# Performance work log

Measured on AMD Instinct MI355X. Metric: run time of the kernel, lower is better.

## Reference

```python
import jax, jax.numpy as jnp
import numpy as np

B, H, S, D = 2, 16, 2048, 64


def setup_inputs() -> dict:
    key = jax.random.key(0)
    kq, kk, kv = jax.random.split(key, 3)
    q = jax.random.normal(kq, (B, H, S, D), dtype=jnp.float32)
    k = jax.random.normal(kk, (B, H, S, D), dtype=jnp.float32)
    v = jax.random.normal(kv, (B, H, S, D), dtype=jnp.float32)
    # causal mask: 1.0 where attention is DISALLOWED (strictly upper triangle)
    mask = jnp.triu(jnp.ones((S, S), dtype=jnp.float32), k=1)[None, None, :, :]
    return {"k": k, "q": q, "v": v, "mask": mask}


def reference(k, q, v, mask):
    d_k = jnp.asarray(k.shape[-1], dtype=jnp.float32)
    # scores: [B, H, S, S]
    scores = jnp.einsum("bhqd,bhkd->bhqk", q, k) / jnp.sqrt(d_k)
    scores = scores + mask * (-1e9)
    weights = jax.nn.softmax(scores, axis=-1)
    # attention output: [B, H, S, D]
    return jnp.einsum("bhqk,bhkd->bhqd", weights, v)
```

## Files before the change

kernel.cpp:

```cpp
#include <hip/hip_runtime.h>
#include <hip/hip_bf16.h>

typedef unsigned short ushort_t;
typedef __attribute__((ext_vector_type(8))) short v8s;
typedef __attribute__((ext_vector_type(4))) float v4f;

#define SEQ   2048
#define DH    64
#define BK    32
#define KSTR  72
#define VSTR  40
#define NHEADS 32
#define GBYTES 19456
#define HELEMS 131072

#if __has_builtin(__builtin_amdgcn_exp2f)
#define EXP2(x) __builtin_amdgcn_exp2f(x)
#else
#define EXP2(x) exp2f(x)
#endif

__device__ __forceinline__ unsigned pkbf(float lo, float hi) {
    __hip_bfloat162 h = __float22bfloat162_rn(make_float2(lo, hi));
    union { __hip_bfloat162 h; unsigned u; } c; c.h = h; return c.u;
}

__device__ __forceinline__ v8s load8_bf_scaled(const float* p, float sc) {
    float4 a = *(const float4*)p;
    float4 b = *(const float4*)(p + 4);
    union { v8s v; unsigned u[4]; } t;
    t.u[0] = pkbf(a.x * sc, a.y * sc);
    t.u[1] = pkbf(a.z * sc, a.w * sc);
    t.u[2] = pkbf(b.x * sc, b.y * sc);
    t.u[3] = pkbf(b.z * sc, b.w * sc);
    return t.v;
}

__device__ __forceinline__ void process_tile_T(
    int kb, int myq0, int quad, int l15,
    v8s qa0, v8s qa1,
    v8s ka00, v8s ka01, v8s ka10, v8s ka11,
    v8s vb0, v8s vb1, v8s vb2, v8s vb3,
    v4f& a0, v4f& a1, v4f& a2, v4f& a3, float& ls)
{
    const v4f z = {0.f, 0.f, 0.f, 0.f};
    __builtin_amdgcn_s_setprio(1);
    v4f s0 = __builtin_amdgcn_mfma_f32_16x16x32_bf16(ka00, qa0, z, 0, 0, 0);
    s0     = __builtin_amdgcn_mfma_f32_16x16x32_bf16(ka01, qa1, s0, 0, 0, 0);
    v4f s1 = __builtin_amdgcn_mfma_f32_16x16x32_bf16(ka10, qa0, z, 0, 0, 0);
    s1     = __builtin_amdgcn_mfma_f32_16x16x32_bf16(ka11, qa1, s1, 0, 0, 0);
    __builtin_amdgcn_s_setprio(0);

    float p0[4], p1[4];
    if (kb + BK <= myq0) {
        #pragma unroll
        for (int r = 0; r < 4; ++r) { p0[r] = EXP2(s0[r]); p1[r] = EXP2(s1[r]); }
    } else {
        const int qrow = myq0 + l15;
        #pragma unroll
        for (int r = 0; r < 4; ++r) {
            p0[r] = (kb + 4 * quad + r      <= qrow) ? EXP2(s0[r]) : 0.f;
            p1[r] = (kb + 16 + 4 * quad + r <= qrow) ? EXP2(s1[r]) : 0.f;
        }
    }
    #pragma unroll
    for (int r = 0; r < 4; ++r) ls += p0[r] + p1[r];

    union { v8s v; unsigned u[4]; } pa;
    pa.u[0] = pkbf(p0[0], p0[1]); pa.u[1] = pkbf(p0[2], p0[3]);
    pa.u[2] = pkbf(p1[0], p1[1]); pa.u[3] = pkbf(p1[2], p1[3]);
    __builtin_amdgcn_s_setprio(1);
    a0 = __builtin_amdgcn_mfma_f32_16x16x32_bf16(pa.v, vb0, a0, 0, 0, 0);
    a1 = __builtin_amdgcn_mfma_f32_16x16x32_bf16(pa.v, vb1, a1, 0, 0, 0);
    a2 = __builtin_amdgcn_mfma_f32_16x16x32_bf16(pa.v, vb2, a2, 0, 0, 0);
    a3 = __builtin_amdgcn_mfma_f32_16x16x32_bf16(pa.v, vb3, a3, 0, 0, 0);
    __builtin_amdgcn_s_setprio(0);
}

__global__ __launch_bounds__(256, 8)
void attn_prep(const float* __restrict__ K, const float* __restrict__ V,
               ushort_t* __restrict__ Kb, ushort_t* __restrict__ Vb) {
    const int u = blockIdx.x * 256 + threadIdx.x;
    if (u < 524288) {
        const float* src = K + (size_t)u * 8;
        float4 a = *(const float4*)src;
        float4 b = *(const float4*)(src + 4);
        union { v8s v; unsigned w[4]; } t;
        t.w[0] = pkbf(a.x, a.y); t.w[1] = pkbf(a.z, a.w);
        t.w[2] = pkbf(b.x, b.y); t.w[3] = pkbf(b.z, b.w);
        *(v8s*)(Kb + (size_t)u * 8) = t.v;
    } else {
        const int q    = u - 524288;
        const int d    = q & 63;
        const int sgrp = (q >> 6) & 3;
        const int tile = (q >> 8) & 63;
        const int head = q >> 14;
        const float* vsrc = V + ((size_t)head * SEQ + tile * 32) * DH + d;
        float x[8];
        #pragma unroll
        for (int m = 0; m < 8; ++m) {
            const int kpos = (m < 4) ? (4 * sgrp + m) : (16 + 4 * sgrp + (m - 4));
            x[m] = vsrc[(size_t)kpos * DH];
        }
        union { v8s v; unsigned w[4]; } t;
        t.w[0] = pkbf(x[0], x[1]); t.w[1] = pkbf(x[2], x[3]);
        t.w[2] = pkbf(x[4], x[5]); t.w[3] = pkbf(x[6], x[7]);
        *(v8s*)(Vb + (size_t)q * 8) = t.v;
    }
}

__global__ __launch_bounds__(512, 4)
void attn_causal_dual2(const ushort_t* __restrict__ Kb,
                       const float* __restrict__ Qg,
                       const ushort_t* __restrict__ Vb,
                       float* __restrict__ Og) {
    __shared__ alignas(16) unsigned char smem[2][GBYTES];

    const int i    = blockIdx.x;
    const int head = i & 31;
    const int j    = i >> 5;
    const int qt   = (j < 16) ? (31 - j) : (j - 16);
    const int qb   = qt * 64;
    const int tid  = threadIdx.x;
    const int w    = tid >> 6;
    const int grp  = w >> 2;
    const int wg   = w & 3;
    const int lane = tid & 63;
    const int l15  = lane & 15;
    const int quad = lane >> 4;

    const int niter = qt + 1;
    const int ktlo  = grp ? niter : 0;

    const int myq0 = qb + wg * 16, qmax = myq0 + 15;
    const size_t hb = (size_t)head * SEQ * DH;

    const float QSC = 0.125f * 1.4426950408889634f;
    v8s qa0, qa1;
    {
        const float* qp = Qg + hb + (size_t)(myq0 + l15) * DH + quad * 8;
        qa0 = load8_bf_scaled(qp, QSC);  qa1 = load8_bf_scaled(qp + 32, QSC);
    }

    v4f a0 = {0.f,0.f,0.f,0.f}, a1 = a0, a2 = a0, a3 = a0;
    float ls = 0.f;

    const int stid    = tid & 255;
    const int sk_kpos = stid >> 3;
    const int sk_d    = (stid & 7) * 8;
    const int sv_d    = stid & 63;
    const int sv_g    = stid >> 6;

    const ushort_t* ksrc = Kb + (size_t)head * HELEMS + stid * 8;
    const ushort_t* vsrc = Vb + (size_t)head * HELEMS + stid * 8;

    ushort_t* KtB = (ushort_t*)(smem[grp]);
    ushort_t* VtB = (ushort_t*)(smem[grp] + 9216);
    ushort_t* kdst0 = KtB + sk_kpos * KSTR + sk_d;
    ushort_t* vdst0 = VtB + sv_d * VSTR + sv_g * 8;
    const int KOFS = BK * KSTR;
    const int VOFS = DH * VSTR;

    {
        union { v8s v; uint4 u; } kc, vc;
        kc.u = *(const uint4*)(ksrc + (size_t)ktlo * 2048);
        vc.u = *(const uint4*)(vsrc + (size_t)ktlo * 2048);
        *(v8s*)kdst0 = kc.v;
        *(v8s*)vdst0 = vc.v;
    }
    __syncthreads();

    for (int it = 0; it < niter; ++it) {
        const int kt  = ktlo + it;
        const int cur = it & 1;
        const bool havenext = (it + 1 < niter);

        uint4 nk, nv;
        if (havenext) {
            nk = *(const uint4*)(ksrc + (size_t)(kt + 1) * 2048);
            nv = *(const uint4*)(vsrc + (size_t)(kt + 1) * 2048);
        }

        const int kb = kt * BK;
        if (kb <= qmax) {
            const ushort_t* KB = KtB + (cur ? KOFS : 0);
            const ushort_t* VB = VtB + (cur ? VOFS : 0);
            union { v8s v; uint4 u; } ka00, ka01, ka10, ka11, vb0, vb1, vb2, vb3;
            ka00.u = *(const uint4*)&KB[(l15)      * KSTR      + quad * 8];
            ka01.u = *(const uint4*)&KB[(l15)      * KSTR + 32 + quad * 8];
            ka10.u = *(const uint4*)&KB[(16 + l15) * KSTR      + quad * 8];
            ka11.u = *(const uint4*)&KB[(16 + l15) * KSTR + 32 + quad * 8];
            vb0.u  = *(const uint4*)&VB[(l15)      * VSTR + quad * 8];
            vb1.u  = *(const uint4*)&VB[(16 + l15) * VSTR + quad * 8];
            vb2.u  = *(const uint4*)&VB[(32 + l15) * VSTR + quad * 8];
            vb3.u  = *(const uint4*)&VB[(48 + l15) * VSTR + quad * 8];

            process_tile_T(kb, myq0, quad, l15, qa0, qa1,
                           ka00.v, ka01.v, ka10.v, ka11.v,
                           vb0.v, vb1.v, vb2.v, vb3.v,
                           a0, a1, a2, a3, ls);
        }

        if (havenext) {
            union { v8s v; uint4 u; } kc, vc;
            kc.u = nk; vc.u = nv;
            const int nxt = cur ^ 1;
            *(v8s*)(kdst0 + (nxt ? KOFS : 0)) = kc.v;
            *(v8s*)(vdst0 + (nxt ? VOFS : 0)) = vc.v;
        }

        __syncthreads();
    }

    ls += __shfl_xor(ls, 16); ls += __shfl_xor(ls, 32);

    float* Ps = (float*)smem[0];
    float* Lp = (float*)smem[1];
    if (grp == 1) {
        #pragma unroll
        for (int r = 0; r < 4; ++r) {
            const int row = wg * 16 + 4 * quad + r;
            float* pr = Ps + row * 68 + l15;
            pr[0] = a0[r]; pr[16] = a1[r]; pr[32] = a2[r]; pr[48] = a3[r];
        }
        if (lane < 16) Lp[wg * 16 + l15] = ls;
    }
    __syncthreads();
    if (grp == 0) {
        const float lst = ls + Lp[wg * 16 + l15];
        #pragma unroll
        for (int r = 0; r < 4; ++r) {
            const float inv = 1.0f / __shfl(lst, 4 * quad + r);
            const int row = wg * 16 + 4 * quad + r;
            const float* pr = Ps + row * 68 + l15;
            float* op = Og + hb + (size_t)(qb + row) * DH + l15;
            op[0]  = (a0[r] + pr[0])  * inv;
            op[16] = (a1[r] + pr[16]) * inv;
            op[32] = (a2[r] + pr[32]) * inv;
            op[48] = (a3[r] + pr[48]) * inv;
        }
    }
}

__global__ __launch_bounds__(512, 4)
void attn_causal_dual(const float* __restrict__ Kg,
                      const float* __restrict__ Qg,
                      const float* __restrict__ Vg,
                      float* __restrict__ Og) {
    __shared__ alignas(16) unsigned char smem[2][GBYTES];

    const int i    = blockIdx.x;
    const int head = i & 31;
    const int j    = i >> 5;
    const int qt   = (j < 16) ? (31 - j) : (j - 16);
    const int qb   = qt * 64;
    const int tid  = threadIdx.x;
    const int w    = tid >> 6;
    const int grp  = w >> 2;
    const int wg   = w & 3;
    const int lane = tid & 63;
    const int l15  = lane & 15;
    const int quad = lane >> 4;

    const int niter = qt + 1;
    const int ktlo  = grp ? niter : 0;

    const int myq0 = qb + wg * 16, qmax = myq0 + 15;
    const size_t hb = (size_t)head * SEQ * DH;

    const float QSC = 0.125f * 1.4426950408889634f;
    v8s qa0, qa1;
    {
        const float* qp = Qg + hb + (size_t)(myq0 + l15) * DH + quad * 8;
        qa0 = load8_bf_scaled(qp, QSC);  qa1 = load8_bf_scaled(qp + 32, QSC);
    }

    v4f a0 = {0.f,0.f,0.f,0.f}, a1 = a0, a2 = a0, a3 = a0;
    float ls = 0.f;

    const int stid    = tid & 255;
    const int sk_kpos = stid >> 3;
    const int sk_d    = (stid & 7) * 8;
    const int sv_d    = stid & 63;

    const float* kbase  = Kg + hb + (size_t)sk_kpos * DH + sk_d;
    const float* vbaseA = Vg + hb + (size_t)(4 * wg) * DH + sv_d;
    const float* vbaseB = Vg + hb + (size_t)(16 + 4 * wg) * DH + sv_d;

    ushort_t* KtB = (ushort_t*)(smem[grp]);
    ushort_t* VtB = (ushort_t*)(smem[grp] + 9216);
    ushort_t* kdst0 = KtB + sk_kpos * KSTR + sk_d;
    ushort_t* vdst0 = VtB + sv_d * VSTR + 8 * wg;
    const int KOFS = BK * KSTR;
    const int VOFS = DH * VSTR;

    {
        const size_t t0 = (size_t)ktlo * BK * DH;
        float4 k0 = *(const float4*)(kbase + t0);
        float4 k1 = *(const float4*)(kbase + t0 + 4);
        float va[4], vb[4];
        #pragma unroll
        for (int m = 0; m < 4; ++m) {
            va[m] = vbaseA[t0 + (size_t)m * DH];
            vb[m] = vbaseB[t0 + (size_t)m * DH];
        }
        union { v8s v; unsigned u[4]; } kc, vc;
        kc.u[0] = pkbf(k0.x, k0.y); kc.u[1] = pkbf(k0.z, k0.w);
        kc.u[2] = pkbf(k1.x, k1.y); kc.u[3] = pkbf(k1.z, k1.w);
        vc.u[0] = pkbf(va[0], va[1]); vc.u[1] = pkbf(va[2], va[3]);
        vc.u[2] = pkbf(vb[0], vb[1]); vc.u[3] = pkbf(vb[2], vb[3]);
        *(v8s*)kdst0 = kc.v;
        *(v8s*)vdst0 = vc.v;
    }
    __syncthreads();

    for (int it = 0; it < niter; ++it) {
        const int kt  = ktlo + it;
        const int cur = it & 1;
        const bool havenext = (it + 1 < niter);

        float4 nk0, nk1; float nva[4], nvb[4];
        if (havenext) {
            const size_t toff = (size_t)(kt + 1) * BK * DH;
            nk0 = *(const float4*)(kbase + toff);
            nk1 = *(const float4*)(kbase + toff + 4);
            #pragma unroll
            for (int m = 0; m < 4; ++m) {
                nva[m] = vbaseA[toff + (size_t)m * DH];
                nvb[m] = vbaseB[toff + (size_t)m * DH];
            }
        }

        const int kb = kt * BK;
        if (kb <= qmax) {
            const ushort_t* KB = KtB + (cur ? KOFS : 0);
            const ushort_t* VB = VtB + (cur ? VOFS : 0);
            union { v8s v; uint4 u; } ka00, ka01, ka10, ka11, vb0, vb1, vb2, vb3;
            ka00.u = *(const uint4*)&KB[(l15)      * KSTR      + quad * 8];
            ka01.u = *(const uint4*)&KB[(l15)      * KSTR + 32 + quad * 8];
            ka10.u = *(const uint4*)&KB[(16 + l15) * KSTR      + quad * 8];
            ka11.u = *(const uint4*)&KB[(16 + l15) * KSTR + 32 + quad * 8];
            vb0.u  = *(const uint4*)&VB[(l15)      * VSTR + quad * 8];
            vb1.u  = *(const uint4*)&VB[(16 + l15) * VSTR + quad * 8];
            vb2.u  = *(const uint4*)&VB[(32 + l15) * VSTR + quad * 8];
            vb3.u  = *(const uint4*)&VB[(48 + l15) * VSTR + quad * 8];

            process_tile_T(kb, myq0, quad, l15, qa0, qa1,
                           ka00.v, ka01.v, ka10.v, ka11.v,
                           vb0.v, vb1.v, vb2.v, vb3.v,
                           a0, a1, a2, a3, ls);
        }

        if (havenext) {
            union { v8s v; unsigned u[4]; } kc, vc;
            kc.u[0] = pkbf(nk0.x, nk0.y); kc.u[1] = pkbf(nk0.z, nk0.w);
            kc.u[2] = pkbf(nk1.x, nk1.y); kc.u[3] = pkbf(nk1.z, nk1.w);
            vc.u[0] = pkbf(nva[0], nva[1]); vc.u[1] = pkbf(nva[2], nva[3]);
            vc.u[2] = pkbf(nvb[0], nvb[1]); vc.u[3] = pkbf(nvb[2], nvb[3]);
            const int nxt = cur ^ 1;
            *(v8s*)(kdst0 + (nxt ? KOFS : 0)) = kc.v;
            *(v8s*)(vdst0 + (nxt ? VOFS : 0)) = vc.v;
        }

        __syncthreads();
    }

    ls += __shfl_xor(ls, 16); ls += __shfl_xor(ls, 32);

    float* Ps = (float*)smem[0];
    float* Lp = (float*)smem[1];
    if (grp == 1) {
        #pragma unroll
        for (int r = 0; r < 4; ++r) {
            const int row = wg * 16 + 4 * quad + r;
            float* pr = Ps + row * 68 + l15;
            pr[0] = a0[r]; pr[16] = a1[r]; pr[32] = a2[r]; pr[48] = a3[r];
        }
        if (lane < 16) Lp[wg * 16 + l15] = ls;
    }
    __syncthreads();
    if (grp == 0) {
        const float lst = ls + Lp[wg * 16 + l15];
        #pragma unroll
        for (int r = 0; r < 4; ++r) {
            const float inv = 1.0f / __shfl(lst, 4 * quad + r);
            const int row = wg * 16 + 4 * quad + r;
            const float* pr = Ps + row * 68 + l15;
            float* op = Og + hb + (size_t)(qb + row) * DH + l15;
            op[0]  = (a0[r] + pr[0])  * inv;
            op[16] = (a1[r] + pr[16]) * inv;
            op[32] = (a2[r] + pr[32]) * inv;
            op[48] = (a3[r] + pr[48]) * inv;
        }
    }
}

extern "C" void kernel_launch(void* const* d_in, const int* in_sizes, int n_in,
                              void* d_out, int out_size, void* d_ws, size_t ws_size,
                              hipStream_t stream) {
    const float* K = (const float*)d_in[0];
    const float* Q = (const float*)d_in[1];
    const float* V = (const float*)d_in[2];
    float* O = (float*)d_out;

    const size_t img_elems = (size_t)NHEADS * HELEMS;
    const size_t need = 2 * img_elems * sizeof(ushort_t);

    if (ws_size >= need) {
        ushort_t* Kb = (ushort_t*)d_ws;
        ushort_t* Vb = Kb + img_elems;
        attn_prep<<<dim3(4096), 256, 0, stream>>>(K, V, Kb, Vb);
        attn_causal_dual2<<<dim3(1024), 512, 0, stream>>>(Kb, Q, Vb, O);
    } else {
        attn_causal_dual<<<dim3(1024), 512, 0, stream>>>(K, Q, V, O);
    }
}
```

Baseline: 140.4 us.

## Load pre-swizzled bf16 K/V fragments directly from global, drop LDS staging

The new main kernel has each wave read its MFMA K and V operand fragments straight from the pre-laid-out bf16 workspace in global memory. This removes the double-buffered LDS staging and the per-tile __syncthreads. Each wave also now stops at its own causal limit instead of iterating with the block's bound. The cost is that K/V data shared across the four waves of a group is re-read from global/L2 instead of once per block, and no explicit prefetch overlaps the loads with compute.

```diff
diff --git a/kernel.cpp b/kernel.cpp
--- a/kernel.cpp
+++ b/kernel.cpp
@@ -110,11 +110,12 @@
 }
 
 __global__ __launch_bounds__(512, 4)
-void attn_causal_dual2(const ushort_t* __restrict__ Kb,
+void attn_causal_dual3(const ushort_t* __restrict__ Kb,
                        const float* __restrict__ Qg,
                        const ushort_t* __restrict__ Vb,
                        float* __restrict__ Og) {
-    __shared__ alignas(16) unsigned char smem[2][GBYTES];
+    __shared__ alignas(16) float Ps[64 * 68];
+    __shared__ float Lp[64];
 
     const int i    = blockIdx.x;
     const int head = i & 31;
@@ -133,6 +134,10 @@
     const int ktlo  = grp ? niter : 0;
 
     const int myq0 = qb + wg * 16, qmax = myq0 + 15;
+    const int kthiN = ktlo + niter;
+    const int kthiC = (qmax >> 5) + 1;
+    const int kthi  = (kthiN < kthiC) ? kthiN : kthiC;
+
     const size_t hb = (size_t)head * SEQ * DH;
 
     const float QSC = 0.125f * 1.4426950408889634f;
@@ -145,26 +150,123 @@
     v4f a0 = {0.f,0.f,0.f,0.f}, a1 = a0, a2 = a0, a3 = a0;
     float ls = 0.f;
 
+    const ushort_t* kh = Kb + (size_t)head * HELEMS + l15 * 64 + quad * 8;
+    const ushort_t* vh = Vb + (size_t)head * HELEMS + quad * 512 + l15 * 8;
+
+    for (int kt = ktlo; kt < kthi; ++kt) {
+        const ushort_t* kp = kh + (size_t)kt * 2048;
+        const ushort_t* vp = vh + (size_t)kt * 2048;
+        union { v8s v; uint4 u; } ka00, ka01, ka10, ka11, vb0, vb1, vb2, vb3;
+        ka00.u = *(const uint4*)(kp);
+        ka01.u = *(const uint4*)(kp + 32);
+        ka10.u = *(const uint4*)(kp + 1024);
+        ka11.u = *(const uint4*)(kp + 1056);
+        vb0.u  = *(const uint4*)(vp);
+        vb1.u  = *(const uint4*)(vp + 128);
+        vb2.u  = *(const uint4*)(vp + 256);
+        vb3.u  = *(const uint4*)(vp + 384);
+
+        process_tile_T(kt * BK, myq0, quad, l15, qa0, qa1,
+                       ka00.v, ka01.v, ka10.v, ka11.v,
+                       vb0.v, vb1.v, vb2.v, vb3.v,
+                       a0, a1, a2, a3, ls);
+    }
+
+    ls += __shfl_xor(ls, 16); ls += __shfl_xor(ls, 32);
+
+    if (grp == 1) {
+        #pragma unroll
+        for (int r = 0; r < 4; ++r) {
+            const int row = wg * 16 + 4 * quad + r;
+            float* pr = Ps + row * 68 + l15;
+            pr[0] = a0[r]; pr[16] = a1[r]; pr[32] = a2[r]; pr[48] = a3[r];
+        }
+        if (lane < 16) Lp[wg * 16 + l15] = ls;
+    }
+    __syncthreads();
+    if (grp == 0) {
+        const float lst = ls + Lp[wg * 16 + l15];
+        #pragma unroll
+        for (int r = 0; r < 4; ++r) {
+            const float inv = 1.0f / __shfl(lst, 4 * quad + r);
+            const int row = wg * 16 + 4 * quad + r;
+            const float* pr = Ps + row * 68 + l15;
+            float* op = Og + hb + (size_t)(qb + row) * DH + l15;
+            op[0]  = (a0[r] + pr[0])  * inv;
+            op[16] = (a1[r] + pr[16]) * inv;
+            op[32] = (a2[r] + pr[32]) * inv;
+            op[48] = (a3[r] + pr[48]) * inv;
+        }
+    }
+}
+
+__global__ __launch_bounds__(512, 4)
+void attn_causal_dual(const float* __restrict__ Kg,
+                      const float* __restrict__ Qg,
+                      const float* __restrict__ Vg,
+                      float* __restrict__ Og) {
+    __shared__ alignas(16) unsigned char smem[2][GBYTES];
+
+    const int i    = blockIdx.x;
+    const int head = i & 31;
+    const int j    = i >> 5;
+    const int qt   = (j < 16) ? (31 - j) : (j - 16);
+    const int qb   = qt * 64;
+    const int tid  = threadIdx.x;
+    const int w    = tid >> 6;
+    const int grp  = w >> 2;
+    const int wg   = w & 3;
+    const int lane = tid & 63;
+    const int l15  = lane & 15;
+    const int quad = lane >> 4;
+
+    const int niter = qt + 1;
+    const int ktlo  = grp ? niter : 0;
+
+    const int myq0 = qb + wg * 16, qmax = myq0 + 15;
+    const size_t hb = (size_t)head * SEQ * DH;
+
+    const float QSC = 0.125f * 1.4426950408889634f;
+    v8s qa0, qa1;
+    {
+        const float* qp = Qg + hb + (size_t)(myq0 + l15) * DH + quad * 8;
+        qa0 = load8_bf_scaled(qp, QSC);  qa1 = load8_bf_scaled(qp + 32, QSC);
+    }
+
+    v4f a0 = {0.f,0.f,0.f,0.f}, a1 = a0, a2 = a0, a3 = a0;
+    float ls = 0.f;
+
     const int stid    = tid & 255;
     const int sk_kpos = stid >> 3;
     const int sk_d    = (stid & 7) * 8;
     const int sv_d    = stid & 63;
-    const int sv_g    = stid >> 6;
-
-    const ushort_t* ksrc = Kb + (size_t)head * HELEMS + stid * 8;
-    const ushort_t* vsrc = Vb + (size_t)head * HELEMS + stid * 8;
+
+    const float* kbase  = Kg + hb + (size_t)sk_kpos * DH + sk_d;
+    const float* vbaseA = Vg + hb + (size_t)(4 * wg) * DH + sv_d;
+    const float* vbaseB = Vg + hb + (size_t)(16 + 4 * wg) * DH + sv_d;
 
     ushort_t* KtB = (ushort_t*)(smem[grp]);
     ushort_t* VtB = (ushort_t*)(smem[grp] + 9216);
     ushort_t* kdst0 = KtB + sk_kpos * KSTR + sk_d;
-    ushort_t* vdst0 = VtB + sv_d * VSTR + sv_g * 8;
+    ushort_t* vdst0 = VtB + sv_d * VSTR + 8 * wg;
     const int KOFS = BK * KSTR;
     const int VOFS = DH * VSTR;
 
     {
-        union { v8s v; uint4 u; } kc, vc;
-        kc.u = *(const uint4*)(ksrc + (size_t)ktlo * 2048);
-        vc.u = *(const uint4*)(vsrc + (size_t)ktlo * 2048);
+        const size_t t0 = (size_t)ktlo * BK * DH;
+        float4 k0 = *(const float4*)(kbase + t0);
+        float4 k1 = *(const float4*)(kbase + t0 + 4);
+        float va[4], vb[4];
+        #pragma unroll
+        for (int m = 0; m < 4; ++m) {
+            va[m] = vbaseA[t0 + (size_t)m * DH];
+            vb[m] = vbaseB[t0 + (size_t)m * DH];
+        }
+        union { v8s v; unsigned u[4]; } kc, vc;
+        kc.u[0] = pkbf(k0.x, k0.y); kc.u[1] = pkbf(k0.z, k0.w);
+        kc.u[2] = pkbf(k1.x, k1.y); kc.u[3] = pkbf(k1.z, k1.w);
+        vc.u[0] = pkbf(va[0], va[1]); vc.u[1] = pkbf(va[2], va[3]);
+        vc.u[2] = pkbf(vb[0], vb[1]); vc.u[3] = pkbf(vb[2], vb[3]);
         *(v8s*)kdst0 = kc.v;
         *(v8s*)vdst0 = vc.v;
     }
@@ -175,10 +277,16 @@
         const int cur = it & 1;
         const bool havenext = (it + 1 < niter);
 
-        uint4 nk, nv;
+        float4 nk0, nk1; float nva[4], nvb[4];
         if (havenext) {
-            nk = *(const uint4*)(ksrc + (size_t)(kt + 1) * 2048);
-            nv = *(const uint4*)(vsrc + (size_t)(kt + 1) * 2048);
+            const size_t toff = (size_t)(kt + 1) * BK * DH;
+            nk0 = *(const float4*)(kbase + toff);
+            nk1 = *(const float4*)(kbase + toff + 4);
+            #pragma unroll
+            for (int m = 0; m < 4; ++m) {
+                nva[m] = vbaseA[toff + (size_t)m * DH];
+                nvb[m] = vbaseB[toff + (size_t)m * DH];
+            }
         }
 
         const int kb = kt * BK;
@@ -202,156 +310,6 @@
         }
 
         if (havenext) {
-            union { v8s v; uint4 u; } kc, vc;
-            kc.u = nk; vc.u = nv;
-            const int nxt = cur ^ 1;
-            *(v8s*)(kdst0 + (nxt ? KOFS : 0)) = kc.v;
-            *(v8s*)(vdst0 + (nxt ? VOFS : 0)) = vc.v;
-        }
-
-        __syncthreads();
-    }
-
-    ls += __shfl_xor(ls, 16); ls += __shfl_xor(ls, 32);
-
-    float* Ps = (float*)smem[0];
-    float* Lp = (float*)smem[1];
-    if (grp == 1) {
-        #pragma unroll
-        for (int r = 0; r < 4; ++r) {
-            const int row = wg * 16 + 4 * quad + r;
-            float* pr = Ps + row * 68 + l15;
-            pr[0] = a0[r]; pr[16] = a1[r]; pr[32] = a2[r]; pr[48] = a3[r];
-        }
-        if (lane < 16) Lp[wg * 16 + l15] = ls;
-    }
-    __syncthreads();
-    if (grp == 0) {
-        const float lst = ls + Lp[wg * 16 + l15];
-        #pragma unroll
-        for (int r = 0; r < 4; ++r) {
-            const float inv = 1.0f / __shfl(lst, 4 * quad + r);
-            const int row = wg * 16 + 4 * quad + r;
-            const float* pr = Ps + row * 68 + l15;
-            float* op = Og + hb + (size_t)(qb + row) * DH + l15;
-            op[0]  = (a0[r] + pr[0])  * inv;
-            op[16] = (a1[r] + pr[16]) * inv;
-            op[32] = (a2[r] + pr[32]) * inv;
-            op[48] = (a3[r] + pr[48]) * inv;
-        }
-    }
-}
-
-__global__ __launch_bounds__(512, 4)
-void attn_causal_dual(const float* __restrict__ Kg,
-                      const float* __restrict__ Qg,
-                      const float* __restrict__ Vg,
-                      float* __restrict__ Og) {
-    __shared__ alignas(16) unsigned char smem[2][GBYTES];
-
-    const int i    = blockIdx.x;
-    const int head = i & 31;
-    const int j    = i >> 5;
-    const int qt   = (j < 16) ? (31 - j) : (j - 16);
-    const int qb   = qt * 64;
-    const int tid  = threadIdx.x;
-    const int w    = tid >> 6;
-    const int grp  = w >> 2;
-    const int wg   = w & 3;
-    const int lane = tid & 63;
-    const int l15  = lane & 15;
-    const int quad = lane >> 4;
-
-    const int niter = qt + 1;
-    const int ktlo  = grp ? niter : 0;
-
-    const int myq0 = qb + wg * 16, qmax = myq0 + 15;
-    const size_t hb = (size_t)head * SEQ * DH;
-
-    const float QSC = 0.125f * 1.4426950408889634f;
-    v8s qa0, qa1;
-    {
-        const float* qp = Qg + hb + (size_t)(myq0 + l15) * DH + quad * 8;
-        qa0 = load8_bf_scaled(qp, QSC);  qa1 = load8_bf_scaled(qp + 32, QSC);
-    }
-
-    v4f a0 = {0.f,0.f,0.f,0.f}, a1 = a0, a2 = a0, a3 = a0;
-    float ls = 0.f;
-
-    const int stid    = tid & 255;
-    const int sk_kpos = stid >> 3;
-    const int sk_d    = (stid & 7) * 8;
-    const int sv_d    = stid & 63;
-
-    const float* kbase  = Kg + hb + (size_t)sk_kpos * DH + sk_d;
-    const float* vbaseA = Vg + hb + (size_t)(4 * wg) * DH + sv_d;
-    const float* vbaseB = Vg + hb + (size_t)(16 + 4 * wg) * DH + sv_d;
-
-    ushort_t* KtB = (ushort_t*)(smem[grp]);
-    ushort_t* VtB = (ushort_t*)(smem[grp] + 9216);
-    ushort_t* kdst0 = KtB + sk_kpos * KSTR + sk_d;
-    ushort_t* vdst0 = VtB + sv_d * VSTR + 8 * wg;
-    const int KOFS = BK * KSTR;
-    const int VOFS = DH * VSTR;
-
-    {
-        const size_t t0 = (size_t)ktlo * BK * DH;
-        float4 k0 = *(const float4*)(kbase + t0);
-        float4 k1 = *(const float4*)(kbase + t0 + 4);
-        float va[4], vb[4];
-        #pragma unroll
-        for (int m = 0; m < 4; ++m) {
-            va[m] = vbaseA[t0 + (size_t)m * DH];
-            vb[m] = vbaseB[t0 + (size_t)m * DH];
-        }
-        union { v8s v; unsigned u[4]; } kc, vc;
-        kc.u[0] = pkbf(k0.x, k0.y); kc.u[1] = pkbf(k0.z, k0.w);
-        kc.u[2] = pkbf(k1.x, k1.y); kc.u[3] = pkbf(k1.z, k1.w);
-        vc.u[0] = pkbf(va[0], va[1]); vc.u[1] = pkbf(va[2], va[3]);
-        vc.u[2] = pkbf(vb[0], vb[1]); vc.u[3] = pkbf(vb[2], vb[3]);
-        *(v8s*)kdst0 = kc.v;
-        *(v8s*)vdst0 = vc.v;
-    }
-    __syncthreads();
-
-    for (int it = 0; it < niter; ++it) {
-        const int kt  = ktlo + it;
-        const int cur = it & 1;
-        const bool havenext = (it + 1 < niter);
-
-        float4 nk0, nk1; float nva[4], nvb[4];
-        if (havenext) {
-            const size_t toff = (size_t)(kt + 1) * BK * DH;
-            nk0 = *(const float4*)(kbase + toff);
-            nk1 = *(const float4*)(kbase + toff + 4);
-            #pragma unroll
-            for (int m = 0; m < 4; ++m) {
-                nva[m] = vbaseA[toff + (size_t)m * DH];
-                nvb[m] = vbaseB[toff + (size_t)m * DH];
-            }
-        }
-
-        const int kb = kt * BK;
-        if (kb <= qmax) {
-            const ushort_t* KB = KtB + (cur ? KOFS : 0);
-            const ushort_t* VB = VtB + (cur ? VOFS : 0);
-            union { v8s v; uint4 u; } ka00, ka01, ka10, ka11, vb0, vb1, vb2, vb3;
-            ka00.u = *(const uint4*)&KB[(l15)      * KSTR      + quad * 8];
-            ka01.u = *(const uint4*)&KB[(l15)      * KSTR + 32 + quad * 8];
-            ka10.u = *(const uint4*)&KB[(16 + l15) * KSTR      + quad * 8];
-            ka11.u = *(const uint4*)&KB[(16 + l15) * KSTR + 32 + quad * 8];
-            vb0.u  = *(const uint4*)&VB[(l15)      * VSTR + quad * 8];
-            vb1.u  = *(const uint4*)&VB[(16 + l15) * VSTR + quad * 8];
-            vb2.u  = *(const uint4*)&VB[(32 + l15) * VSTR + quad * 8];
-            vb3.u  = *(const uint4*)&VB[(48 + l15) * VSTR + quad * 8];
-
-            process_tile_T(kb, myq0, quad, l15, qa0, qa1,
-                           ka00.v, ka01.v, ka10.v, ka11.v,
-                           vb0.v, vb1.v, vb2.v, vb3.v,
-                           a0, a1, a2, a3, ls);
-        }
-
-        if (havenext) {
             union { v8s v; unsigned u[4]; } kc, vc;
             kc.u[0] = pkbf(nk0.x, nk0.y); kc.u[1] = pkbf(nk0.z, nk0.w);
             kc.u[2] = pkbf(nk1.x, nk1.y); kc.u[3] = pkbf(nk1.z, nk1.w);
@@ -367,25 +325,25 @@
 
     ls += __shfl_xor(ls, 16); ls += __shfl_xor(ls, 32);
 
-    float* Ps = (float*)smem[0];
-    float* Lp = (float*)smem[1];
+    float* Ps2 = (float*)smem[0];
+    float* Lp2 = (float*)smem[1];
     if (grp == 1) {
         #pragma unroll
         for (int r = 0; r < 4; ++r) {
             const int row = wg * 16 + 4 * quad + r;
-            float* pr = Ps + row * 68 + l15;
+            float* pr = Ps2 + row * 68 + l15;
             pr[0] = a0[r]; pr[16] = a1[r]; pr[32] = a2[r]; pr[48] = a3[r];
         }
-        if (lane < 16) Lp[wg * 16 + l15] = ls;
+        if (lane < 16) Lp2[wg * 16 + l15] = ls;
     }
     __syncthreads();
     if (grp == 0) {
-        const float lst = ls + Lp[wg * 16 + l15];
+        const float lst = ls + Lp2[wg * 16 + l15];
         #pragma unroll
         for (int r = 0; r < 4; ++r) {
             const float inv = 1.0f / __shfl(lst, 4 * quad + r);
             const int row = wg * 16 + 4 * quad + r;
-            const float* pr = Ps + row * 68 + l15;
+            const float* pr = Ps2 + row * 68 + l15;
             float* op = Og + hb + (size_t)(qb + row) * DH + l15;
             op[0]  = (a0[r] + pr[0])  * inv;
             op[16] = (a1[r] + pr[16]) * inv;
@@ -410,7 +368,7 @@
         ushort_t* Kb = (ushort_t*)d_ws;
         ushort_t* Vb = Kb + img_elems;
         attn_prep<<<dim3(4096), 256, 0, stream>>>(K, V, Kb, Vb);
-        attn_causal_dual2<<<dim3(1024), 512, 0, stream>>>(Kb, Q, Vb, O);
+        attn_causal_dual3<<<dim3(1024), 512, 0, stream>>>(Kb, Q, Vb, O);
     } else {
         attn_causal_dual<<<dim3(1024), 512, 0, stream>>>(K, Q, V, O);
     }
```

New measurement: 198.4 us. +41.3%, slower.
